# Optimization experiments

Hardware: AMD Instinct MI355X
Metric: run time of the kernel (lower is better)

Reference implementation:

```python
import jax, jax.numpy as jnp
import numpy as np

N_ENT = 50000
N_EDGE = 500000
H_DIM = 128
N_REL_TAB = 475  # 2*n_rel + 1


def setup_inputs() -> dict:
    key = jax.random.key(0)
    ks = jax.random.split(key, 8)
    scale = 1.0 / np.sqrt(H_DIM)
    return {
        "ent_emb": jax.random.normal(ks[0], (N_ENT, H_DIM), jnp.float32) * scale,
        "rel_emb": jax.random.normal(ks[1], (N_REL_TAB, H_DIM), jnp.float32) * scale,
        "w_edge": jax.random.normal(ks[2], (H_DIM, H_DIM), jnp.float32) * scale,
        "w_node": jax.random.normal(ks[3], (H_DIM, H_DIM), jnp.float32) * scale,
        "w_comp": jax.random.normal(ks[4], (H_DIM, H_DIM), jnp.float32) * scale,
        "src": jax.random.randint(ks[5], (N_EDGE,), 0, N_ENT, jnp.int32),
        "dst": jax.random.randint(ks[6], (N_EDGE,), 0, N_ENT, jnp.int32),
        "rel_id": jax.random.randint(ks[7], (N_EDGE,), 0, N_REL_TAB - 1, jnp.int32),
    }


def _edge_softmax(logits, dst, n_nodes):
    # dgl.ops.edge_softmax: softmax over incoming edges of each destination node
    m = jax.ops.segment_max(logits, dst, num_segments=n_nodes)  # (N,)
    ex = jnp.exp(logits - m[dst])                               # (E,)
    s = jax.ops.segment_sum(ex, dst, num_segments=n_nodes)     # (N,)
    return ex / s[dst]


def _attn_aggregate(msg, key_emb_dst, dst, n_nodes, w):
    # norm = e_dot_v, edge_softmax, weighted scatter-sum, GEMM, Tanh
    logits = jnp.sum(msg * key_emb_dst, axis=-1)                # (E,)
    a = _edge_softmax(logits, dst, n_nodes)                     # (E,)
    neigh = jax.ops.segment_sum(msg * a[:, None], dst, num_segments=n_nodes)  # (N,H)
    return jnp.tanh(neigh @ w)


def reference(ent_emb, rel_emb, w_edge, w_node, w_comp, src, dst, rel_id):
    n = ent_emb.shape[0]
    v = ent_emb[dst]            # (E,H) destination node emb (shared key for all layers)
    u = ent_emb[src]            # (E,H)
    r = rel_emb[rel_id]         # (E,H)

    # EdgeLayer: message = rel emb
    edge_out = _attn_aggregate(r, v, dst, n, w_edge)
    # NodeLayer: message = src node emb (u_dot_v logits, u_mul_e aggregation)
    node_out = _attn_aggregate(u, v, dst, n, w_node)
    # CompLayer (comp_op='add'): message = u + rel emb
    comp_out = _attn_aggregate(u + r, v, dst, n, w_comp)

    return ent_emb + edge_out + node_out + comp_out
```

## Files before the change

### kernel.cpp

```cpp
#include <hip/hip_runtime.h>
#include <math.h>

#define N_ENT   50000
#define N_REL   475
#define N_EDGE  500000
#define HD      128

typedef unsigned int u32;
typedef __attribute__((ext_vector_type(8))) short short8;
typedef __attribute__((ext_vector_type(4))) float f32x4;
typedef __attribute__((ext_vector_type(2))) float f32x2;
typedef __attribute__((ext_vector_type(4))) u32 u32x4;

__device__ __forceinline__ u32 bf16_1(float f) {
  u32 u = __float_as_uint(f);
  return (u + 0x7fffu + ((u >> 16) & 1u)) >> 16;
}
__device__ __forceinline__ u32 bf16_pack(float lo, float hi) {
  return bf16_1(lo) | (bf16_1(hi) << 16);
}
__device__ __forceinline__ float bf_lo(u32 w) { return __uint_as_float(w << 16); }
__device__ __forceinline__ float bf_hi(u32 w) { return __uint_as_float(w & 0xffff0000u); }
__device__ __forceinline__ f32x2 bf2(u32 w) { return (f32x2){bf_lo(w), bf_hi(w)}; }
__device__ __forceinline__ float fast_tanh(float x) {
  float e = __expf(2.f * x);
  return 1.f - 2.f * __builtin_amdgcn_rcpf(e + 1.f);
}

#define DEG_BLKS ((N_EDGE + 255) / 256)
#define CVT_ITEMS ((N_ENT + N_REL) * 16 + 3 * 8 * 4 * 64)
#define CVT_BLKS ((CVT_ITEMS + 255) / 256)

__global__ void k_degree_cvt(const int* __restrict__ dst, int* __restrict__ counts,
                             const float* __restrict__ ent, const float* __restrict__ rel,
                             const float* __restrict__ we, const float* __restrict__ wn,
                             const float* __restrict__ wc, u32* __restrict__ ent16,
                             u32* __restrict__ rel16, u32* __restrict__ wpack) {
  int b = blockIdx.x;
  if (b < DEG_BLKS) {
    int e = b * 256 + threadIdx.x;
    if (e < N_EDGE) atomicAdd(&counts[dst[e]], 1);
    return;
  }
  int t = (b - DEG_BLKS) * 256 + threadIdx.x;
  const int CVT = (N_ENT + N_REL) * 16;
  if (t < CVT) {
    int row = t >> 4, seg = t & 15;
    const float* s;
    u32* d;
    if (row < N_ENT) {
      s = ent + (size_t)row * HD + seg * 8;
      d = ent16 + (size_t)row * 64 + seg * 4;
    } else {
      int rr = row - N_ENT;
      s = rel + (size_t)rr * HD + seg * 8;
      d = rel16 + (size_t)rr * 64 + seg * 4;
    }
    float4 A = *(const float4*)s, B = *(const float4*)(s + 4);
    u32x4 o = {bf16_pack(A.x, A.y), bf16_pack(A.z, A.w),
               bf16_pack(B.x, B.y), bf16_pack(B.z, B.w)};
    *(u32x4*)d = o;
  } else if (t < CVT_ITEMS) {
    int idx = t - CVT;
    int lane = idx & 63, ks = (idx >> 6) & 3, ct = (idx >> 8) & 7, l = idx >> 11;
    const float* W = (l == 0) ? we : (l == 1) ? wn : wc;
    int c = ct * 16 + (lane & 15);
    int kb = ks * 32 + (lane >> 4) * 8;
    u32x4 o;
#pragma unroll
    for (int jp = 0; jp < 4; ++jp) {
      int k0 = kb + 2 * jp;
      o[jp] = bf16_pack(W[k0 * HD + c], W[(k0 + 1) * HD + c]);
    }
    *(u32x4*)(wpack + idx * 4) = o;
  }
}

__global__ void k_blocksum(const int* __restrict__ counts, int* __restrict__ bsum) {
  __shared__ int sh[256];
  int i = blockIdx.x * 256 + threadIdx.x;
  sh[threadIdx.x] = (i < N_ENT) ? counts[i] : 0;
  __syncthreads();
  for (int off = 128; off > 0; off >>= 1) {
    if (threadIdx.x < off) sh[threadIdx.x] += sh[threadIdx.x + off];
    __syncthreads();
  }
  if (threadIdx.x == 0) bsum[blockIdx.x] = sh[0];
}

__global__ void k_scan_top(int* __restrict__ bsum, int nb) {
  __shared__ int sh[256];
  int t = threadIdx.x;
  int v = (t < nb) ? bsum[t] : 0;
  sh[t] = v;
  __syncthreads();
  for (int off = 1; off < 256; off <<= 1) {
    int x = (t >= off) ? sh[t - off] : 0;
    __syncthreads();
    sh[t] += x;
    __syncthreads();
  }
  if (t < nb) bsum[t] = sh[t] - v;
}

__global__ void k_scan_final(const int* __restrict__ counts, const int* __restrict__ bsum,
                             int* __restrict__ row_ptr) {
  __shared__ int sh[256];
  int t = threadIdx.x;
  int i = blockIdx.x * 256 + t;
  int v = (i < N_ENT) ? counts[i] : 0;
  sh[t] = v;
  __syncthreads();
  for (int off = 1; off < 256; off <<= 1) {
    int x = (t >= off) ? sh[t - off] : 0;
    __syncthreads();
    sh[t] += x;
    __syncthreads();
  }
  if (i < N_ENT) row_ptr[i] = sh[t] - v + bsum[blockIdx.x];
  if (i == N_ENT - 1) row_ptr[N_ENT] = N_EDGE;
}

__global__ void k_scatter(const int* __restrict__ src, const int* __restrict__ dst,
                          const int* __restrict__ rel, const int* __restrict__ row_ptr,
                          int* __restrict__ cursor, u32* __restrict__ psru) {
  int e = blockIdx.x * 256 + threadIdx.x;
  if (e >= N_EDGE) return;
  int d = dst[e];
  int pos = row_ptr[d] + atomicAdd(&cursor[d], 1);
  psru[pos] = (u32)src[e] | ((u32)rel[e] << 16);
}

__global__ __launch_bounds__(256) void k_aggregate(
    const u32* __restrict__ ent16, const u32* __restrict__ rel16,
    const int* __restrict__ row_ptr, const u32* __restrict__ psru,
    u32* __restrict__ neighb) {
  int lane = threadIdx.x & 63;
  int node = blockIdx.x * 4 + (threadIdx.x >> 6);
  int grp = lane >> 4, gl = lane & 15;

  u32x4 V = *(const u32x4*)(ent16 + (size_t)node * 64 + gl * 4);
  f32x2 vv2[4];
#pragma unroll
  for (int k = 0; k < 4; ++k) vv2[k] = bf2(V[k]);

  f32x2 Su = {0.f, 0.f};
  float S2 = 0.f;
  f32x2 a0[4], a1[4], a2[4];
#pragma unroll
  for (int k = 0; k < 4; ++k) a0[k] = a1[k] = a2[k] = (f32x2){0.f, 0.f};

  int e0 = row_ptr[node], e1 = row_ptr[node + 1];
  if (e0 < e1) {
    int elast = e1 - 1;
    auto fetch = [&](int eb, u32x4& U, u32x4& R) {
      int e = eb + grp;
      u32 p = psru[(e < e1) ? e : elast];
      U = *(const u32x4*)(ent16 + (size_t)(p & 0xFFFFu) * 64 + gl * 4);
      R = *(const u32x4*)(rel16 + (size_t)(p >> 16) * 64 + gl * 4);
    };
    auto process = [&](u32x4& U, u32x4& R, int eb) {
      f32x2 cu2[4], cr2[4];
#pragma unroll
      for (int k = 0; k < 4; ++k) { cu2[k] = bf2(U[k]); cr2[k] = bf2(R[k]); }
      fetch(eb + 12, U, R);
      bool valid = (eb + grp < e1);
      f32x2 du2 = {0.f, 0.f}, dq2 = {0.f, 0.f};
#pragma unroll
      for (int k = 0; k < 4; ++k) {
        du2 += cu2[k] * vv2[k];
        dq2 += cr2[k] * vv2[k];
      }
      f32x2 p = {du2.x + du2.y, dq2.x + dq2.y};
#pragma unroll
      for (int off = 1; off < 16; off <<= 1) {
        f32x2 t;
        t.x = __shfl_xor(p.x, off, 64);
        t.y = __shfl_xor(p.y, off, 64);
        p += t;
      }
      float e_u = valid ? __expf(p.x) : 0.f;
      float e_r = valid ? __expf(p.y) : 0.f;
      float e_c = e_u * e_r;
      Su += (f32x2){e_r, e_u};
      S2 += e_c;
      f32x2 er2 = {e_r, e_r}, eu2 = {e_u, e_u}, ec2 = {e_c, e_c};
#pragma unroll
      for (int k = 0; k < 4; ++k) {
        a0[k] += er2 * cr2[k];
        a1[k] += eu2 * cu2[k];
        a2[k] += ec2 * (cu2[k] + cr2[k]);
      }
    };
    u32x4 uA, rA, uB, rB, uC, rC;
    fetch(e0, uA, rA);
    fetch(e0 + 4, uB, rB);
    fetch(e0 + 8, uC, rC);
    int eb = e0;
    for (; eb + 8 < e1; eb += 12) {
      process(uA, rA, eb);
      process(uB, rB, eb + 4);
      process(uC, rC, eb + 8);
    }
    if (eb < e1) process(uA, rA, eb);
    if (eb + 4 < e1) process(uB, rB, eb + 4);
  }

  {
    f32x2 t;
    t.x = __shfl_xor(Su.x, 16, 64); t.y = __shfl_xor(Su.y, 16, 64); Su += t;
    t.x = __shfl_xor(Su.x, 32, 64); t.y = __shfl_xor(Su.y, 32, 64); Su += t;
    S2 += __shfl_xor(S2, 16, 64); S2 += __shfl_xor(S2, 32, 64);
  }
  float w0 = (Su.x > 0.f) ? __builtin_amdgcn_rcpf(Su.x) : 0.f;
  float w1 = (Su.y > 0.f) ? __builtin_amdgcn_rcpf(Su.y) : 0.f;
  float w2 = (S2 > 0.f) ? __builtin_amdgcn_rcpf(S2) : 0.f;
#pragma unroll
  for (int k = 0; k < 4; ++k) {
    f32x2 t;
    t.x = __shfl_xor(a0[k].x, 16, 64); t.y = __shfl_xor(a0[k].y, 16, 64); a0[k] += t;
    t.x = __shfl_xor(a0[k].x, 32, 64); t.y = __shfl_xor(a0[k].y, 32, 64); a0[k] += t;
    t.x = __shfl_xor(a1[k].x, 16, 64); t.y = __shfl_xor(a1[k].y, 16, 64); a1[k] += t;
    t.x = __shfl_xor(a1[k].x, 32, 64); t.y = __shfl_xor(a1[k].y, 32, 64); a1[k] += t;
    t.x = __shfl_xor(a2[k].x, 16, 64); t.y = __shfl_xor(a2[k].y, 16, 64); a2[k] += t;
    t.x = __shfl_xor(a2[k].x, 32, 64); t.y = __shfl_xor(a2[k].y, 32, 64); a2[k] += t;
  }

  int base = node * 64 + gl * 4;
  if (grp == 0) {
    u32x4 o = {bf16_pack(a0[0].x * w0, a0[0].y * w0), bf16_pack(a0[1].x * w0, a0[1].y * w0),
               bf16_pack(a0[2].x * w0, a0[2].y * w0), bf16_pack(a0[3].x * w0, a0[3].y * w0)};
    *(u32x4*)(neighb + base) = o;
  } else if (grp == 1) {
    u32x4 o = {bf16_pack(a1[0].x * w1, a1[0].y * w1), bf16_pack(a1[1].x * w1, a1[1].y * w1),
               bf16_pack(a1[2].x * w1, a1[2].y * w1), bf16_pack(a1[3].x * w1, a1[3].y * w1)};
    *(u32x4*)(neighb + N_ENT * 64 + base) = o;
  } else if (grp == 2) {
    u32x4 o = {bf16_pack(a2[0].x * w2, a2[0].y * w2), bf16_pack(a2[1].x * w2, a2[1].y * w2),
               bf16_pack(a2[2].x * w2, a2[2].y * w2), bf16_pack(a2[3].x * w2, a2[3].y * w2)};
    *(u32x4*)(neighb + 2 * N_ENT * 64 + base) = o;
  }
}

__global__ __launch_bounds__(256) void k_out(
    const float* __restrict__ ent, const u32* __restrict__ neighb,
    const u32* __restrict__ wpack, float* __restrict__ out) {
  int lane = threadIdx.x & 63, wv = threadIdx.x >> 6;
  int n0 = blockIdx.x * 64 + wv * 16;

  int arow = n0 + (lane & 15);
  int arow_c = (arow < N_ENT) ? arow : 0;
  int ko2 = (lane >> 4) * 4;

  f32x4 res[8];
#pragma unroll
  for (int t = 0; t < 8; ++t) res[t] = (f32x4){0.f, 0.f, 0.f, 0.f};

#pragma unroll
  for (int l = 0; l < 3; ++l) {
    const u32* nb = neighb + (size_t)l * N_ENT * 64;
    short8 a[4];
#pragma unroll
    for (int ks = 0; ks < 4; ++ks)
      a[ks] = *(const short8*)(nb + (size_t)arow_c * 64 + ks * 16 + ko2);
    const u32* wp = wpack + l * 8192;
#pragma unroll
    for (int ct = 0; ct < 8; ++ct) {
      f32x4 acc = (f32x4){0.f, 0.f, 0.f, 0.f};
#pragma unroll
      for (int ks = 0; ks < 4; ++ks) {
        short8 b = *(const short8*)(wp + ((ct * 4 + ks) * 64 + lane) * 4);
        acc = __builtin_amdgcn_mfma_f32_16x16x32_bf16(a[ks], b, acc, 0, 0, 0);
      }
#pragma unroll
      for (int r = 0; r < 4; ++r) res[ct][r] += fast_tanh(acc[r]);
    }
  }
  int rbase = n0 + (lane >> 4) * 4;
  int cbase = lane & 15;
#pragma unroll
  for (int ct = 0; ct < 8; ++ct) {
    int col = ct * 16 + cbase;
#pragma unroll
    for (int r = 0; r < 4; ++r) {
      int row = rbase + r;
      if (row < N_ENT)
        out[(size_t)row * HD + col] = ent[(size_t)row * HD + col] + res[ct][r];
    }
  }
}

extern "C" void kernel_launch(void* const* d_in, const int* in_sizes, int n_in,
                              void* d_out, int out_size, void* d_ws, size_t ws_size,
                              hipStream_t stream) {
  const float* ent = (const float*)d_in[0];
  const float* rel = (const float*)d_in[1];
  const float* w_e = (const float*)d_in[2];
  const float* w_n = (const float*)d_in[3];
  const float* w_c = (const float*)d_in[4];
  const int* src = (const int*)d_in[5];
  const int* dst = (const int*)d_in[6];
  const int* relid = (const int*)d_in[7];
  float* out = (float*)d_out;

  char* ws = (char*)d_ws;
  size_t off = 0;
  auto alloc = [&](size_t bytes) {
    void* p = ws + off;
    off = (off + bytes + 255) & ~(size_t)255;
    return p;
  };
  int* counts = (int*)alloc((size_t)N_ENT * 4);
  int* cursor = (int*)alloc((size_t)N_ENT * 4);
  int* row_ptr = (int*)alloc((size_t)(N_ENT + 1) * 4);
  int* bsum = (int*)alloc(256 * 4);
  u32* psru = (u32*)alloc((size_t)N_EDGE * 4);
  u32* ent16 = (u32*)alloc((size_t)N_ENT * 64 * 4);
  u32* rel16 = (u32*)alloc((size_t)N_REL * 64 * 4);
  u32* neighb = (u32*)alloc(3ull * N_ENT * 64 * 4);
  u32* wpack = (u32*)alloc((size_t)3 * 8 * 4 * 64 * 4 * 4);
  (void)ws_size; (void)in_sizes; (void)n_in; (void)out_size;

  hipMemsetAsync(counts, 0, (size_t)((char*)row_ptr - (char*)counts), stream);

  int nb = (N_ENT + 255) / 256;
  k_degree_cvt<<<DEG_BLKS + CVT_BLKS, 256, 0, stream>>>(dst, counts, ent, rel, w_e, w_n,
                                                        w_c, ent16, rel16, wpack);
  k_blocksum<<<nb, 256, 0, stream>>>(counts, bsum);
  k_scan_top<<<1, 256, 0, stream>>>(bsum, nb);
  k_scan_final<<<nb, 256, 0, stream>>>(counts, bsum, row_ptr);
  k_scatter<<<(N_EDGE + 255) / 256, 256, 0, stream>>>(src, dst, relid, row_ptr, cursor,
                                                      psru);
  k_aggregate<<<N_ENT / 4, 256, 0, stream>>>(ent16, rel16, row_ptr, psru, neighb);
  k_out<<<(N_ENT + 63) / 64, 256, 0, stream>>>(ent, neighb, wpack, out);
}
```

Baseline: 241.4 us.

## Fuse three-pass scan into single-pass chained scan; stage GEMM A-tile via LDS

Replaces the blocksum/scan_top/scan_final kernels with one kernel where each block waits on its predecessor's inclusive prefix published through a flag-tagged 64-bit chain entry, removing two launches and their gaps. The chain buffer is zeroed by the existing memset. The output GEMM now loads neighbour rows with coalesced 16-byte reads into a padded LDS slab before forming MFMA A fragments, instead of strided global reads. The chained scan relies on blocks being scheduled roughly in order and serialises the 196 blocks through a spin loop.

```diff
diff --git a/kernel.cpp b/kernel.cpp
--- a/kernel.cpp
+++ b/kernel.cpp
@@ -7,6 +7,7 @@
 #define HD      128
 
 typedef unsigned int u32;
+typedef unsigned long long u64;
 typedef __attribute__((ext_vector_type(8))) short short8;
 typedef __attribute__((ext_vector_type(4))) float f32x4;
 typedef __attribute__((ext_vector_type(2))) float f32x2;
@@ -30,6 +31,7 @@
 #define DEG_BLKS ((N_EDGE + 255) / 256)
 #define CVT_ITEMS ((N_ENT + N_REL) * 16 + 3 * 8 * 4 * 64)
 #define CVT_BLKS ((CVT_ITEMS + 255) / 256)
+#define SCAN_BLKS ((N_ENT + 255) / 256)
 
 __global__ void k_degree_cvt(const int* __restrict__ dst, int* __restrict__ counts,
                              const float* __restrict__ ent, const float* __restrict__ rel,
@@ -76,38 +78,13 @@
   }
 }
 
-__global__ void k_blocksum(const int* __restrict__ counts, int* __restrict__ bsum) {
+__global__ __launch_bounds__(256) void k_scan(const int* __restrict__ counts,
+                                              int* __restrict__ row_ptr,
+                                              u64* __restrict__ chain) {
   __shared__ int sh[256];
-  int i = blockIdx.x * 256 + threadIdx.x;
-  sh[threadIdx.x] = (i < N_ENT) ? counts[i] : 0;
-  __syncthreads();
-  for (int off = 128; off > 0; off >>= 1) {
-    if (threadIdx.x < off) sh[threadIdx.x] += sh[threadIdx.x + off];
-    __syncthreads();
-  }
-  if (threadIdx.x == 0) bsum[blockIdx.x] = sh[0];
-}
-
-__global__ void k_scan_top(int* __restrict__ bsum, int nb) {
-  __shared__ int sh[256];
-  int t = threadIdx.x;
-  int v = (t < nb) ? bsum[t] : 0;
-  sh[t] = v;
-  __syncthreads();
-  for (int off = 1; off < 256; off <<= 1) {
-    int x = (t >= off) ? sh[t - off] : 0;
-    __syncthreads();
-    sh[t] += x;
-    __syncthreads();
-  }
-  if (t < nb) bsum[t] = sh[t] - v;
-}
-
-__global__ void k_scan_final(const int* __restrict__ counts, const int* __restrict__ bsum,
-                             int* __restrict__ row_ptr) {
-  __shared__ int sh[256];
-  int t = threadIdx.x;
-  int i = blockIdx.x * 256 + t;
+  __shared__ int s_prefix;
+  int t = threadIdx.x, b = blockIdx.x;
+  int i = b * 256 + t;
   int v = (i < N_ENT) ? counts[i] : 0;
   sh[t] = v;
   __syncthreads();
@@ -117,7 +94,18 @@
     sh[t] += x;
     __syncthreads();
   }
-  if (i < N_ENT) row_ptr[i] = sh[t] - v + bsum[blockIdx.x];
+  if (t == 255) {
+    u64 pre = 0;
+    if (b > 0) {
+      u64 w;
+      do { w = atomicAdd(&chain[b - 1], 0ull); } while ((w >> 32) == 0);
+      pre = w & 0xffffffffull;
+    }
+    atomicExch(&chain[b], (1ull << 32) | (pre + (u64)(u32)sh[255]));
+    s_prefix = (int)pre;
+  }
+  __syncthreads();
+  if (i < N_ENT) row_ptr[i] = s_prefix + sh[t] - v;
   if (i == N_ENT - 1) row_ptr[N_ENT] = N_EDGE;
 }
 
@@ -245,12 +233,10 @@
 __global__ __launch_bounds__(256) void k_out(
     const float* __restrict__ ent, const u32* __restrict__ neighb,
     const u32* __restrict__ wpack, float* __restrict__ out) {
+  __shared__ u32 lds[4][16 * 68];
   int lane = threadIdx.x & 63, wv = threadIdx.x >> 6;
   int n0 = blockIdx.x * 64 + wv * 16;
-
-  int arow = n0 + (lane & 15);
-  int arow_c = (arow < N_ENT) ? arow : 0;
-  int ko2 = (lane >> 4) * 4;
+  u32* slab = &lds[wv][0];
 
   f32x4 res[8];
 #pragma unroll
@@ -258,11 +244,19 @@
 
 #pragma unroll
   for (int l = 0; l < 3; ++l) {
-    const u32* nb = neighb + (size_t)l * N_ENT * 64;
+    const u32* nb = neighb + (size_t)l * (N_ENT * 64);
+#pragma unroll
+    for (int i = 0; i < 4; ++i) {
+      int nrel = 4 * i + (lane >> 4);
+      int nidx = n0 + nrel;
+      if (nidx >= N_ENT) nidx = N_ENT - 1;
+      u32x4 vls = *(const u32x4*)(nb + (size_t)nidx * 64 + (lane & 15) * 4);
+      *(u32x4*)(slab + nrel * 68 + (lane & 15) * 4) = vls;
+    }
     short8 a[4];
 #pragma unroll
     for (int ks = 0; ks < 4; ++ks)
-      a[ks] = *(const short8*)(nb + (size_t)arow_c * 64 + ks * 16 + ko2);
+      a[ks] = *(const short8*)(slab + (lane & 15) * 68 + ks * 16 + (lane >> 4) * 4);
     const u32* wp = wpack + l * 8192;
 #pragma unroll
     for (int ct = 0; ct < 8; ++ct) {
@@ -312,8 +306,8 @@
   };
   int* counts = (int*)alloc((size_t)N_ENT * 4);
   int* cursor = (int*)alloc((size_t)N_ENT * 4);
+  u64* chain = (u64*)alloc((size_t)SCAN_BLKS * 8);
   int* row_ptr = (int*)alloc((size_t)(N_ENT + 1) * 4);
-  int* bsum = (int*)alloc(256 * 4);
   u32* psru = (u32*)alloc((size_t)N_EDGE * 4);
   u32* ent16 = (u32*)alloc((size_t)N_ENT * 64 * 4);
   u32* rel16 = (u32*)alloc((size_t)N_REL * 64 * 4);
@@ -323,12 +317,9 @@
 
   hipMemsetAsync(counts, 0, (size_t)((char*)row_ptr - (char*)counts), stream);
 
-  int nb = (N_ENT + 255) / 256;
   k_degree_cvt<<<DEG_BLKS + CVT_BLKS, 256, 0, stream>>>(dst, counts, ent, rel, w_e, w_n,
                                                         w_c, ent16, rel16, wpack);
-  k_blocksum<<<nb, 256, 0, stream>>>(counts, bsum);
-  k_scan_top<<<1, 256, 0, stream>>>(bsum, nb);
-  k_scan_final<<<nb, 256, 0, stream>>>(counts, bsum, row_ptr);
+  k_scan<<<SCAN_BLKS, 256, 0, stream>>>(counts, row_ptr, chain);
   k_scatter<<<(N_EDGE + 255) / 256, 256, 0, stream>>>(src, dst, relid, row_ptr, cursor,
                                                       psru);
   k_aggregate<<<N_ENT / 4, 256, 0, stream>>>(ent16, rel16, row_ptr, psru, neighb);
```

Result: slower. 379.5 us (+57.2%).
